# Performance work log

Hardware: AMD Instinct MI355X
Metric: run time of the kernel (lower is better)

The kernel has to match this reference:

```python
import jax, jax.numpy as jnp
import numpy as np

B, S, H, R, N = 8, 4096, 1024, 128, 256
A_LOGIT_INIT = 6.906754778648554      # logit(0.999)
DELTA_LOG_INIT = 0.5413248546129181   # log(exp(1.0) - 1.0), softplus^-1(1.0)


def setup_inputs() -> dict:
    key = jax.random.key(0)
    ks = jax.random.split(key, 6)
    x = jax.random.normal(ks[0], (B, S, H), dtype=jnp.float32)
    state0 = jnp.zeros((B, N), dtype=jnp.float32)
    in_basis = jax.random.normal(ks[1], (R, H), dtype=jnp.float32) / np.sqrt(H)
    q_select = jax.random.normal(ks[2], (N, R), dtype=jnp.float32) / np.sqrt(R)
    k_select = jax.random.normal(ks[3], (N, R), dtype=jnp.float32) / np.sqrt(R)
    v_input = jax.random.normal(ks[4], (N, R), dtype=jnp.float32) / np.sqrt(R)
    out_proj = jax.random.normal(ks[5], (H, N), dtype=jnp.float32) / np.sqrt(N)
    a_logit = jnp.full((N,), A_LOGIT_INIT, dtype=jnp.float32)
    delta_log = jnp.full((N,), DELTA_LOG_INIT, dtype=jnp.float32)
    return {"x": x, "state0": state0, "in_basis": in_basis, "q_select": q_select,
            "k_select": k_select, "v_input": v_input, "out_proj": out_proj,
            "a_logit": a_logit, "delta_log": delta_log}


def reference(x, state0, in_basis, q_select, k_select, v_input, out_proj,
              a_logit, delta_log):
    # Projections (all timesteps at once; equivalent to per-step F.linear)
    z = jnp.einsum('bsh,rh->bsr', x, in_basis)          # [B,S,R]
    b = jnp.einsum('bsr,nr->bsn', z, k_select)          # [B,S,N]
    c = jnp.einsum('bsr,nr->bsn', z, q_select)          # [B,S,N]
    v = jnp.einsum('bsr,nr->bsn', z, v_input)           # [B,S,N]

    a = jax.nn.sigmoid(a_logit)                         # [N]
    delta = jax.nn.softplus(delta_log)                  # [N]
    u = delta * (b * v)                                 # [B,S,N] driving input

    # Diagonal linear recurrence: s_t = a * s_{t-1} + u_t ; y_t = c_t * s_t
    u_t = jnp.swapaxes(u, 0, 1)                         # [S,B,N]
    c_t = jnp.swapaxes(c, 0, 1)                         # [S,B,N]

    def step(s, inp):
        u_i, c_i = inp
        s = a * s + u_i
        return s, c_i * s

    final_state, ys = jax.lax.scan(step, state0, (u_t, c_t))  # ys: [S,B,N]
    out = jnp.einsum('sbn,hn->bsh', ys, out_proj)       # [B,S,H]
    return out, final_state
```

## Files before the change

### kernel.cpp

```cpp
#include <hip/hip_runtime.h>
#include <math.h>

#define Bb 8
#define Ss 4096
#define Hh 1024
#define Rr 128
#define Nn 256
#define Mm (Bb*Ss)
#define LCH 128
#define NCHK (Ss/LCH)

typedef __attribute__((ext_vector_type(8))) short bf16x8;
typedef __attribute__((ext_vector_type(4))) float f32x4;

__device__ __forceinline__ float sigmoidf_(float x) { return 1.0f / (1.0f + expf(-x)); }
__device__ __forceinline__ float softplusf_(float x) { return log1pf(expf(x)); }

__device__ __forceinline__ unsigned short f2b(float f) {
    union { float f; unsigned int u; } v; v.f = f;
    return (unsigned short)((v.u + 0x7fffu + ((v.u >> 16) & 1u)) >> 16);
}
__device__ __forceinline__ float b2f(unsigned short h) {
    union { unsigned int u; float f; } v; v.u = ((unsigned int)h) << 16;
    return v.f;
}

__device__ __forceinline__ void gl_lds16(const void* g, void* l) {
    __builtin_amdgcn_global_load_lds(
        (const __attribute__((address_space(1))) void*)g,
        (__attribute__((address_space(3))) void*)l, 16, 0, 0);
}

__global__ __launch_bounds__(256)
void cast_w(const float* __restrict__ s0, const float* __restrict__ s1,
            const float* __restrict__ s2, const float* __restrict__ s3,
            const float* __restrict__ s4,
            unsigned short* __restrict__ d0, unsigned short* __restrict__ d1,
            unsigned short* __restrict__ d2, unsigned short* __restrict__ d3,
            unsigned short* __restrict__ d4)
{
    const int i = blockIdx.x * 256 + threadIdx.x;
    if (i < 131072)      d0[i] = f2b(s0[i]);
    else if (i < 163840) d1[i - 131072] = f2b(s1[i - 131072]);
    else if (i < 196608) d2[i - 163840] = f2b(s2[i - 163840]);
    else if (i < 229376) d3[i - 196608] = f2b(s3[i - 196608]);
    else                 d4[i - 229376] = f2b(s4[i - 229376]);
}

__global__ __launch_bounds__(256)
void g1_fused(const float* __restrict__ X, const unsigned short* __restrict__ IB,
              unsigned short* __restrict__ Z)
{
    __shared__ __align__(16) unsigned short As[64 * 32];
    __shared__ __align__(16) unsigned short Bs[128 * 32];
    const int tid = threadIdx.x;
    const int wave = tid >> 6, lane = tid & 63;
    const int m0 = blockIdx.x * 64;
    const int wm = (wave & 1) * 32, wn = (wave >> 1) * 64;
    const int quad = lane >> 4, lm = lane & 15;
    const int srow = lane >> 2;
    const int skoff = (lane & 3) * 8;
    const int arow = tid >> 3;
    const int akf = (tid & 7) * 4;

    f32x4 acc[2][4] = {};

    for (int k0 = 0; k0 < Hh; k0 += 32) {
#pragma unroll
        for (int q = 0; q < 2; ++q) {
            const int row = q * 32 + arow;
            const float4 v = *(const float4*)(X + (size_t)(m0 + row) * Hh + k0 + akf);
            uint2 o;
            o.x = (unsigned)f2b(v.x) | ((unsigned)f2b(v.y) << 16);
            o.y = (unsigned)f2b(v.z) | ((unsigned)f2b(v.w) << 16);
            *(uint2*)&As[row * 32 + akf] = o;
        }
        gl_lds16(IB + (size_t)(2 * wave * 16 + srow) * Hh + k0 + skoff, &Bs[wave * 1024]);
        gl_lds16(IB + (size_t)((2 * wave + 1) * 16 + srow) * Hh + k0 + skoff, &Bs[wave * 1024 + 512]);
        __syncthreads();
        bf16x8 af[2], bfv[4];
#pragma unroll
        for (int i = 0; i < 2; ++i)
            af[i] = *(const bf16x8*)&As[(wm + i * 16 + lm) * 32 + quad * 8];
#pragma unroll
        for (int j = 0; j < 4; ++j)
            bfv[j] = *(const bf16x8*)&Bs[(wn + j * 16 + lm) * 32 + quad * 8];
#pragma unroll
        for (int i = 0; i < 2; ++i)
#pragma unroll
            for (int j = 0; j < 4; ++j)
                acc[i][j] = __builtin_amdgcn_mfma_f32_16x16x32_bf16(af[i], bfv[j], acc[i][j], 0, 0, 0);
        __syncthreads();
    }

#pragma unroll
    for (int i = 0; i < 2; ++i) {
        const int rbase = m0 + wm + i * 16 + quad * 4;
#pragma unroll
        for (int j = 0; j < 4; ++j) {
            const int col = wn + j * 16 + lm;
#pragma unroll
            for (int r = 0; r < 4; ++r)
                Z[(size_t)(rbase + r) * Rr + col] = f2b(acc[i][j][r]);
        }
    }
}

__global__ __launch_bounds__(256)
void proj_mfma(const unsigned short* __restrict__ Zm, const unsigned short* __restrict__ Kw,
               const unsigned short* __restrict__ Qw, const unsigned short* __restrict__ Vw,
               const float* __restrict__ delta_log, const float* __restrict__ a_logit,
               unsigned short* __restrict__ U, unsigned short* __restrict__ C,
               float* __restrict__ Pout)
{
    __shared__ __align__(16) char smem[34816];
    unsigned short* zs = (unsigned short*)smem;
    unsigned short* ks = (unsigned short*)(smem + 8192);
    unsigned short* qs = (unsigned short*)(smem + 12288);
    unsigned short* vs = (unsigned short*)(smem + 16384);
    float* uL = (float*)smem;
    float* pcomb = (float*)(smem + 33792);

    const int tid = threadIdx.x;
    const int wave = tid >> 6, lane = tid & 63;
    const int m0 = blockIdx.x * 128, n0 = blockIdx.y * 64;
    const int wm = (wave & 1) * 64, wn = (wave >> 1) * 32;
    const int quad = lane >> 4, lm = lane & 15;
    const int srow = lane >> 2;
    const int skoff = (lane & 3) * 8;

    f32x4 aB[4][2] = {}, aC[4][2] = {}, aV[4][2] = {};

    for (int k0 = 0; k0 < Rr; k0 += 32) {
        gl_lds16(Zm + (size_t)(m0 + 2 * wave * 16 + srow) * Rr + k0 + skoff, &zs[wave * 1024]);
        gl_lds16(Zm + (size_t)(m0 + (2 * wave + 1) * 16 + srow) * Rr + k0 + skoff, &zs[wave * 1024 + 512]);
        gl_lds16(Kw + (size_t)(n0 + wave * 16 + srow) * Rr + k0 + skoff, &ks[wave * 512]);
        gl_lds16(Qw + (size_t)(n0 + wave * 16 + srow) * Rr + k0 + skoff, &qs[wave * 512]);
        gl_lds16(Vw + (size_t)(n0 + wave * 16 + srow) * Rr + k0 + skoff, &vs[wave * 512]);
        __syncthreads();
        bf16x8 zf[4], wf[2];
#pragma unroll
        for (int i = 0; i < 4; ++i)
            zf[i] = *(const bf16x8*)&zs[(wm + i * 16 + lm) * 32 + quad * 8];
#pragma unroll
        for (int j = 0; j < 2; ++j)
            wf[j] = *(const bf16x8*)&ks[(wn + j * 16 + lm) * 32 + quad * 8];
#pragma unroll
        for (int i = 0; i < 4; ++i)
#pragma unroll
            for (int j = 0; j < 2; ++j)
                aB[i][j] = __builtin_amdgcn_mfma_f32_16x16x32_bf16(zf[i], wf[j], aB[i][j], 0, 0, 0);
#pragma unroll
        for (int j = 0; j < 2; ++j)
            wf[j] = *(const bf16x8*)&qs[(wn + j * 16 + lm) * 32 + quad * 8];
#pragma unroll
        for (int i = 0; i < 4; ++i)
#pragma unroll
            for (int j = 0; j < 2; ++j)
                aC[i][j] = __builtin_amdgcn_mfma_f32_16x16x32_bf16(zf[i], wf[j], aC[i][j], 0, 0, 0);
#pragma unroll
        for (int j = 0; j < 2; ++j)
            wf[j] = *(const bf16x8*)&vs[(wn + j * 16 + lm) * 32 + quad * 8];
#pragma unroll
        for (int i = 0; i < 4; ++i)
#pragma unroll
            for (int j = 0; j < 2; ++j)
                aV[i][j] = __builtin_amdgcn_mfma_f32_16x16x32_bf16(zf[i], wf[j], aV[i][j], 0, 0, 0);
        __syncthreads();
    }

    float dl[2];
#pragma unroll
    for (int j = 0; j < 2; ++j)
        dl[j] = softplusf_(delta_log[n0 + wn + j * 16 + lm]);

#pragma unroll
    for (int i = 0; i < 4; ++i) {
        const int lrow = wm + i * 16 + quad * 4;
        const int rbase = m0 + lrow;
#pragma unroll
        for (int j = 0; j < 2; ++j) {
            const int col = wn + j * 16 + lm;
            const int gcol = n0 + col;
#pragma unroll
            for (int r = 0; r < 4; ++r) {
                const float uval = dl[j] * aB[i][j][r] * aV[i][j][r];
                const size_t idx = (size_t)(rbase + r) * Nn + gcol;
                U[idx] = f2b(uval);
                C[idx] = f2b(aC[i][j][r]);
                uL[(lrow + r) * 66 + col] = uval;
            }
        }
    }
    __syncthreads();

    const int colp = tid & 63, seg = tid >> 6;
    const float a = sigmoidf_(a_logit[n0 + colp]);
    float l = 0.0f;
#pragma unroll 8
    for (int r = 0; r < 32; ++r)
        l = fmaf(a, l, uL[(seg * 32 + r) * 66 + colp]);
    pcomb[seg * 64 + colp] = l;
    __syncthreads();
    if (tid < 64) {
        float a32 = a;
#pragma unroll
        for (int i = 0; i < 5; ++i) a32 *= a32;
        const float Pv = ((pcomb[tid] * a32 + pcomb[64 + tid]) * a32
                          + pcomb[128 + tid]) * a32 + pcomb[192 + tid];
        Pout[(size_t)blockIdx.x * Nn + n0 + tid] = Pv;
    }
}

__global__ __launch_bounds__(256)
void scan_mid(const float* __restrict__ P, const float* __restrict__ state0,
              const float* __restrict__ a_logit,
              float* __restrict__ start, float* __restrict__ final_state)
{
    const int g = blockIdx.x * blockDim.x + threadIdx.x;
    const int n = g & (Nn - 1);
    const int b = g >> 8;
    const float a = sigmoidf_(a_logit[n]);
    float aL = a;
#pragma unroll
    for (int i = 0; i < 7; ++i) aL *= aL;
    float s = state0[g];
#pragma unroll
    for (int ch = 0; ch < NCHK; ++ch) {
        const size_t idx = ((size_t)(b * NCHK + ch)) * Nn + n;
        start[idx] = s;
        s = fmaf(aL, s, P[idx]);
    }
    final_state[g] = s;
}

__global__ __launch_bounds__(256)
void scan_chunk_c(unsigned short* __restrict__ uy, const unsigned short* __restrict__ cm,
                  const float* __restrict__ start, const float* __restrict__ a_logit)
{
    const int g = blockIdx.x * blockDim.x + threadIdx.x;
    const int n = g & (Nn - 1);
    const int rest = g >> 8;
    const int ch = rest & (NCHK - 1);
    const int b = rest >> 5;
    const float a = sigmoidf_(a_logit[n]);
    float s = start[((size_t)(b * NCHK + ch)) * Nn + n];
    size_t idx = ((size_t)(b * Ss + ch * LCH)) * Nn + n;
#pragma unroll 8
    for (int t = 0; t < LCH; ++t) {
        s = fmaf(a, s, b2f(uy[idx]));
        uy[idx] = f2b(b2f(cm[idx]) * s);
        idx += Nn;
    }
}

__global__ __launch_bounds__(256)
void mfma_nt_f32(const unsigned short* __restrict__ A, const unsigned short* __restrict__ B,
                 float* __restrict__ Cout, int M, int N, int K)
{
    __shared__ __align__(16) unsigned short As[128 * 32];
    __shared__ __align__(16) unsigned short Bs[128 * 32];
    const int tid = threadIdx.x;
    const int wave = tid >> 6, lane = tid & 63;
    const int m0 = blockIdx.x * 128, n0 = blockIdx.y * 128;
    const int wm = (wave & 1) * 64, wn = (wave >> 1) * 64;
    const int quad = lane >> 4, lm = lane & 15;
    const int srow = lane >> 2;
    const int skoff = (lane & 3) * 8;
    const int r0 = wave * 2, r1 = r0 + 1;

    f32x4 acc[4][4] = {};

    for (int k0 = 0; k0 < K; k0 += 32) {
        gl_lds16(A + (size_t)(m0 + r0 * 16 + srow) * K + k0 + skoff, &As[r0 * 512]);
        gl_lds16(A + (size_t)(m0 + r1 * 16 + srow) * K + k0 + skoff, &As[r1 * 512]);
        gl_lds16(B + (size_t)(n0 + r0 * 16 + srow) * K + k0 + skoff, &Bs[r0 * 512]);
        gl_lds16(B + (size_t)(n0 + r1 * 16 + srow) * K + k0 + skoff, &Bs[r1 * 512]);
        __syncthreads();
        bf16x8 af[4], bfv[4];
#pragma unroll
        for (int i = 0; i < 4; ++i)
            af[i] = *(const bf16x8*)&As[(wm + i * 16 + lm) * 32 + quad * 8];
#pragma unroll
        for (int j = 0; j < 4; ++j)
            bfv[j] = *(const bf16x8*)&Bs[(wn + j * 16 + lm) * 32 + quad * 8];
#pragma unroll
        for (int i = 0; i < 4; ++i)
#pragma unroll
            for (int j = 0; j < 4; ++j)
                acc[i][j] = __builtin_amdgcn_mfma_f32_16x16x32_bf16(af[i], bfv[j], acc[i][j], 0, 0, 0);
        __syncthreads();
    }

#pragma unroll
    for (int i = 0; i < 4; ++i) {
        const int rbase = m0 + wm + i * 16 + quad * 4;
#pragma unroll
        for (int j = 0; j < 4; ++j) {
            const int col = n0 + wn + j * 16 + lm;
#pragma unroll
            for (int r = 0; r < 4; ++r)
                Cout[(size_t)(rbase + r) * N + col] = acc[i][j][r];
        }
    }
}

extern "C" void kernel_launch(void* const* d_in, const int* in_sizes, int n_in,
                              void* d_out, int out_size, void* d_ws, size_t ws_size,
                              hipStream_t stream)
{
    const float* x         = (const float*)d_in[0];
    const float* state0    = (const float*)d_in[1];
    const float* in_basis  = (const float*)d_in[2];
    const float* q_select  = (const float*)d_in[3];
    const float* k_select  = (const float*)d_in[4];
    const float* v_input   = (const float*)d_in[5];
    const float* out_proj  = (const float*)d_in[6];
    const float* a_logit   = (const float*)d_in[7];
    const float* delta_log = (const float*)d_in[8];

    float* out = (float*)d_out;
    float* final_state = out + (size_t)Mm * Hh;

    char* ws = (char*)d_ws;
    unsigned short* u  = (unsigned short*)ws;
    unsigned short* c  = (unsigned short*)(ws + 16777216);
    unsigned short* zb = (unsigned short*)(ws + 33554432);
    unsigned short* ib = (unsigned short*)(ws + 41943040);
    unsigned short* kb = (unsigned short*)(ws + 42205184);
    unsigned short* qb = (unsigned short*)(ws + 42270720);
    unsigned short* vb = (unsigned short*)(ws + 42336256);
    unsigned short* ob = (unsigned short*)(ws + 42401792);
    float* P  = (float*)(ws + 42926080);
    float* st = (float*)(ws + 43188224);

    cast_w<<<491520 / 256, 256, 0, stream>>>(in_basis, k_select, q_select, v_input, out_proj,
                                             ib, kb, qb, vb, ob);

    g1_fused<<<Mm / 64, 256, 0, stream>>>(x, ib, zb);

    proj_mfma<<<dim3(Mm / 128, Nn / 64), 256, 0, stream>>>(zb, kb, qb, vb,
                                                           delta_log, a_logit, u, c, P);

    scan_mid<<<(Bb * Nn) / 256, 256, 0, stream>>>(P, state0, a_logit, st, final_state);
    scan_chunk_c<<<(Bb * NCHK * Nn) / 256, 256, 0, stream>>>(u, c, st, a_logit);

    mfma_nt_f32<<<dim3(Mm / 128, Hh / 128), 256, 0, stream>>>(u, ob, out, Mm, Hh, Nn);
}
```

Measured before the change: 323.2 us.

## Fuse chunk scan into output projection GEMM via LDS-resident y tile

```diff
diff --git a/kernel.cpp b/kernel.cpp
--- a/kernel.cpp
+++ b/kernel.cpp
@@ -235,72 +235,82 @@
 }
 
 __global__ __launch_bounds__(256)
-void scan_chunk_c(unsigned short* __restrict__ uy, const unsigned short* __restrict__ cm,
-                  const float* __restrict__ start, const float* __restrict__ a_logit)
-{
-    const int g = blockIdx.x * blockDim.x + threadIdx.x;
-    const int n = g & (Nn - 1);
-    const int rest = g >> 8;
-    const int ch = rest & (NCHK - 1);
-    const int b = rest >> 5;
-    const float a = sigmoidf_(a_logit[n]);
-    float s = start[((size_t)(b * NCHK + ch)) * Nn + n];
-    size_t idx = ((size_t)(b * Ss + ch * LCH)) * Nn + n;
-#pragma unroll 8
-    for (int t = 0; t < LCH; ++t) {
-        s = fmaf(a, s, b2f(uy[idx]));
-        uy[idx] = f2b(b2f(cm[idx]) * s);
-        idx += Nn;
-    }
-}
-
-__global__ __launch_bounds__(256)
-void mfma_nt_f32(const unsigned short* __restrict__ A, const unsigned short* __restrict__ B,
-                 float* __restrict__ Cout, int M, int N, int K)
-{
-    __shared__ __align__(16) unsigned short As[128 * 32];
+void scan_g4_fused(const unsigned short* __restrict__ U, const unsigned short* __restrict__ C,
+                   const float* __restrict__ start, const float* __restrict__ a_logit,
+                   const unsigned short* __restrict__ OB, float* __restrict__ Out)
+{
+    __shared__ __align__(16) unsigned short ys[128 * 256];
     __shared__ __align__(16) unsigned short Bs[128 * 32];
     const int tid = threadIdx.x;
     const int wave = tid >> 6, lane = tid & 63;
-    const int m0 = blockIdx.x * 128, n0 = blockIdx.y * 128;
+    const int m0 = blockIdx.x * 128;
+    const int bidx = m0 >> 12;
+    const int ch = (m0 & (Ss - 1)) >> 7;
+
+    if (tid < 128) {
+        const int n = tid * 2;
+        const float a0 = sigmoidf_(a_logit[n]);
+        const float a1 = sigmoidf_(a_logit[n + 1]);
+        const size_t sb = ((size_t)(bidx * NCHK + ch)) * Nn + n;
+        float s0 = start[sb], s1 = start[sb + 1];
+        size_t gb = ((size_t)m0) * Nn + n;
+        const int slot = n >> 3;
+        const int e = n & 7;
+#pragma unroll 8
+        for (int t = 0; t < LCH; ++t) {
+            const unsigned uu = *(const unsigned*)(U + gb);
+            const unsigned cc = *(const unsigned*)(C + gb);
+            s0 = fmaf(a0, s0, b2f((unsigned short)uu));
+            s1 = fmaf(a1, s1, b2f((unsigned short)(uu >> 16)));
+            const float y0 = b2f((unsigned short)cc) * s0;
+            const float y1 = b2f((unsigned short)(cc >> 16)) * s1;
+            *(unsigned*)&ys[t * 256 + (((slot ^ (t & 7)) << 3) + e)] =
+                (unsigned)f2b(y0) | ((unsigned)f2b(y1) << 16);
+            gb += Nn;
+        }
+    }
+
     const int wm = (wave & 1) * 64, wn = (wave >> 1) * 64;
     const int quad = lane >> 4, lm = lane & 15;
     const int srow = lane >> 2;
-    const int skoff = (lane & 3) * 8;
+    const int skoff = (((lane & 3) ^ ((srow >> 1) & 3)) << 3);
     const int r0 = wave * 2, r1 = r0 + 1;
 
-    f32x4 acc[4][4] = {};
-
-    for (int k0 = 0; k0 < K; k0 += 32) {
-        gl_lds16(A + (size_t)(m0 + r0 * 16 + srow) * K + k0 + skoff, &As[r0 * 512]);
-        gl_lds16(A + (size_t)(m0 + r1 * 16 + srow) * K + k0 + skoff, &As[r1 * 512]);
-        gl_lds16(B + (size_t)(n0 + r0 * 16 + srow) * K + k0 + skoff, &Bs[r0 * 512]);
-        gl_lds16(B + (size_t)(n0 + r1 * 16 + srow) * K + k0 + skoff, &Bs[r1 * 512]);
-        __syncthreads();
-        bf16x8 af[4], bfv[4];
-#pragma unroll
-        for (int i = 0; i < 4; ++i)
-            af[i] = *(const bf16x8*)&As[(wm + i * 16 + lm) * 32 + quad * 8];
-#pragma unroll
-        for (int j = 0; j < 4; ++j)
-            bfv[j] = *(const bf16x8*)&Bs[(wn + j * 16 + lm) * 32 + quad * 8];
-#pragma unroll
-        for (int i = 0; i < 4; ++i)
-#pragma unroll
-            for (int j = 0; j < 4; ++j)
-                acc[i][j] = __builtin_amdgcn_mfma_f32_16x16x32_bf16(af[i], bfv[j], acc[i][j], 0, 0, 0);
-        __syncthreads();
-    }
-
-#pragma unroll
-    for (int i = 0; i < 4; ++i) {
-        const int rbase = m0 + wm + i * 16 + quad * 4;
-#pragma unroll
-        for (int j = 0; j < 4; ++j) {
-            const int col = n0 + wn + j * 16 + lm;
-#pragma unroll
-            for (int r = 0; r < 4; ++r)
-                Cout[(size_t)(rbase + r) * N + col] = acc[i][j][r];
+    for (int n0 = 0; n0 < Hh; n0 += 128) {
+        f32x4 acc[4][4] = {};
+        for (int k0 = 0; k0 < Nn; k0 += 32) {
+            gl_lds16(OB + (size_t)(n0 + r0 * 16 + srow) * Nn + k0 + skoff, &Bs[r0 * 512]);
+            gl_lds16(OB + (size_t)(n0 + r1 * 16 + srow) * Nn + k0 + skoff, &Bs[r1 * 512]);
+            __syncthreads();
+            bf16x8 af[4], bfv[4];
+            const int c8 = (k0 >> 3) + quad;
+#pragma unroll
+            for (int i = 0; i < 4; ++i) {
+                const int r = wm + i * 16 + lm;
+                af[i] = *(const bf16x8*)&ys[r * 256 + ((c8 ^ (r & 7)) << 3)];
+            }
+#pragma unroll
+            for (int j = 0; j < 4; ++j) {
+                const int row = wn + j * 16 + lm;
+                bfv[j] = *(const bf16x8*)&Bs[row * 32 + ((quad ^ ((row >> 1) & 3)) << 3)];
+            }
+#pragma unroll
+            for (int i = 0; i < 4; ++i)
+#pragma unroll
+                for (int j = 0; j < 4; ++j)
+                    acc[i][j] = __builtin_amdgcn_mfma_f32_16x16x32_bf16(af[i], bfv[j], acc[i][j], 0, 0, 0);
+            __syncthreads();
+        }
+#pragma unroll
+        for (int i = 0; i < 4; ++i) {
+            const int rbase = m0 + wm + i * 16 + quad * 4;
+#pragma unroll
+            for (int j = 0; j < 4; ++j) {
+                const int col = n0 + wn + j * 16 + lm;
+#pragma unroll
+                for (int r = 0; r < 4; ++r)
+                    Out[(size_t)(rbase + r) * Hh + col] = acc[i][j][r];
+            }
         }
     }
 }
@@ -343,7 +353,6 @@
                                                            delta_log, a_logit, u, c, P);
 
     scan_mid<<<(Bb * Nn) / 256, 256, 0, stream>>>(P, state0, a_logit, st, final_state);
-    scan_chunk_c<<<(Bb * NCHK * Nn) / 256, 256, 0, stream>>>(u, c, st, a_logit);
-
-    mfma_nt_f32<<<dim3(Mm / 128, Hh / 128), 256, 0, stream>>>(u, ob, out, Mm, Hh, Nn);
-}
+
+    scan_g4_fused<<<Mm / 128, 256, 0, stream>>>(u, c, st, a_logit, ob, out);
+}
```

Measured after the change: 334.1 us. 3.4% more time.
